# Performance work log

Hardware: AMD Instinct MI355X
Metric: run time of the kernel (lower is better)

## Reference

```python
import jax, jax.numpy as jnp
import numpy as np

NEG_INF = -1e30


def setup_inputs() -> dict:
    key = jax.random.key(0)
    ks = jax.random.split(key, 5)
    B, S, D, H = 2, 2048, 1024, 16
    sc = 0.02  # weight init scale
    return {
        "x": jax.random.normal(ks[0], (B, S, D), dtype=jnp.float32),
        "Wq": jax.random.normal(ks[1], (D, D), dtype=jnp.float32) * sc,
        "bq": jnp.zeros((D,), dtype=jnp.float32),
        "Wk": jax.random.normal(ks[2], (D, D), dtype=jnp.float32) * sc,
        "bk": jnp.zeros((D,), dtype=jnp.float32),
        "Wv": jax.random.normal(ks[3], (D, D), dtype=jnp.float32) * sc,
        "bv": jnp.zeros((D,), dtype=jnp.float32),
        "Wo": jax.random.normal(ks[4], (D, D), dtype=jnp.float32) * sc,
        "bo": jnp.zeros((D,), dtype=jnp.float32),
        "temperature": jnp.ones((H,), dtype=jnp.float32),
    }


def reference(x, Wq, bq, Wk, bk, Wv, bv, Wo, bo, temperature):
    B, S, D = x.shape
    H = temperature.shape[0]
    hd = D // H
    sparsity = 0.8
    k = max(1, int(S * (1.0 - sparsity)))
    scale = hd ** (-0.5)

    # torch Linear: y = x @ W^T + b ; reshape to [B, S, H, hd] -> [B, H, S, hd]
    def proj(W, b):
        return (x @ W.T + b).reshape(B, S, H, hd).transpose(0, 2, 1, 3)

    q, kk, v = proj(Wq, bq), proj(Wk, bk), proj(Wv, bv)

    temp = jnp.clip(temperature, 0.1, None)[None, :, None, None]  # [1,H,1,1]
    scores = jnp.einsum("bhqd,bhkd->bhqk", q, kk) * scale / temp  # [B,H,S,S]

    # top-k sparsity: keep the k largest scores per row, -inf elsewhere.
    # Equivalent to torch's topk+scatter for distinct values: threshold at
    # the k-th largest value per row.
    topk_vals = jax.lax.top_k(scores, k)[0]           # [B,H,S,k]
    kth = topk_vals[..., -1:]                          # [B,H,S,1]
    sparse_scores = jnp.where(scores >= kth, scores, NEG_INF)

    attn = jax.nn.softmax(sparse_scores, axis=-1)      # [B,H,S,S]
    head_out = jnp.einsum("bhqk,bhkd->bhqd", attn, v)  # [B,H,S,hd]

    # stack heads back: [B,S,H,hd] -> [B,S,D], then out projection
    out = head_out.transpose(0, 2, 1, 3).reshape(B, S, D)
    out = out @ Wo.T + bo

    avg_attention = attn.mean(axis=1)                  # [B,S,S]
    return out, avg_attention
```

## Files before the change

kernel.cpp:

```cpp
#include <hip/hip_runtime.h>
#include <stdint.h>

#define S_LEN 2048
#define D_DIM 1024
#define NHEAD 16
#define HD    64
#define TOPK  409

typedef unsigned short u16;
typedef __attribute__((ext_vector_type(8))) short bf16x8;
typedef __attribute__((ext_vector_type(4))) float f32x4;
#define MFMA __builtin_amdgcn_mfma_f32_16x16x32_bf16

__device__ __forceinline__ u16 f2b(float f) {
    unsigned u = __float_as_uint(f);
    return (u16)((u + 0x7fffu + ((u >> 16) & 1u)) >> 16);
}
__device__ __forceinline__ float b2f(u16 h) {
    return __uint_as_float(((unsigned)h) << 16);
}

__global__ __launch_bounds__(256, 4)
void split_f32(const float* __restrict__ src, u16* __restrict__ hi,
               u16* __restrict__ lo, int n4)
{
    const int i = blockIdx.x * 256 + threadIdx.x;
    if (i >= n4) return;
    const float4 v = ((const float4*)src)[i];
    const float vv[4] = {v.x, v.y, v.z, v.w};
    u16 h4[4], l4[4];
#pragma unroll
    for (int c = 0; c < 4; ++c) {
        h4[c] = f2b(vv[c]);
        l4[c] = f2b(vv[c] - b2f(h4[c]));
    }
    ((ushort4*)hi)[i] = make_ushort4(h4[0], h4[1], h4[2], h4[3]);
    ((ushort4*)lo)[i] = make_ushort4(l4[0], l4[1], l4[2], l4[3]);
}

__global__ __launch_bounds__(256, 4)
void split4_f32(const float* __restrict__ s0, const float* __restrict__ s1,
                const float* __restrict__ s2, const float* __restrict__ s3,
                u16* __restrict__ h0, u16* __restrict__ l0,
                u16* __restrict__ h1, u16* __restrict__ l1,
                u16* __restrict__ h2, u16* __restrict__ l2,
                u16* __restrict__ h3, u16* __restrict__ l3, int n4)
{
    const int i = blockIdx.x * 256 + threadIdx.x;
    if (i >= n4) return;
    const int y = blockIdx.y;
    const float* src = (y == 0) ? s0 : (y == 1) ? s1 : (y == 2) ? s2 : s3;
    u16* hi = (y == 0) ? h0 : (y == 1) ? h1 : (y == 2) ? h2 : h3;
    u16* lo = (y == 0) ? l0 : (y == 1) ? l1 : (y == 2) ? l2 : l3;
    const float4 v = ((const float4*)src)[i];
    const float vv[4] = {v.x, v.y, v.z, v.w};
    u16 h4[4], l4[4];
#pragma unroll
    for (int c = 0; c < 4; ++c) {
        h4[c] = f2b(vv[c]);
        l4[c] = f2b(vv[c] - b2f(h4[c]));
    }
    ((ushort4*)hi)[i] = make_ushort4(h4[0], h4[1], h4[2], h4[3]);
    ((ushort4*)lo)[i] = make_ushort4(l4[0], l4[1], l4[2], l4[3]);
}

template<int MODE>
__global__ __launch_bounds__(512, 2)
void proj_mfma(const u16* __restrict__ Ahi, const u16* __restrict__ Alo,
               const u16* __restrict__ Whi, const u16* __restrict__ Wlo,
               const float* __restrict__ bias, float* __restrict__ outf,
               u16* __restrict__ o1, u16* __restrict__ o2)
{
    const int t = threadIdx.x, w = t >> 6, l = t & 63;
    const int lq = l & 15, quad = l >> 4;
    const int m0 = blockIdx.y * 128 + (w >> 2) * 64;
    const int n0 = blockIdx.x * 128 + (w & 3) * 32;

    f32x4 acc[4][2];
#pragma unroll
    for (int i = 0; i < 4; ++i)
#pragma unroll
        for (int j = 0; j < 2; ++j) acc[i][j] = (f32x4){0.f, 0.f, 0.f, 0.f};

    const size_t abase = (size_t)(m0 + lq) * D_DIM + quad * 8;
    const size_t bbase = (size_t)(n0 + lq) * D_DIM + quad * 8;

#pragma unroll 2
    for (int k0 = 0; k0 < D_DIM; k0 += 32) {
        bf16x8 ah[4], al[4], bh[2], bl[2];
#pragma unroll
        for (int i = 0; i < 4; ++i) {
            ah[i] = *(const bf16x8*)(Ahi + abase + (size_t)i * 16 * D_DIM + k0);
            al[i] = *(const bf16x8*)(Alo + abase + (size_t)i * 16 * D_DIM + k0);
        }
#pragma unroll
        for (int j = 0; j < 2; ++j) {
            bh[j] = *(const bf16x8*)(Whi + bbase + (size_t)j * 16 * D_DIM + k0);
            bl[j] = *(const bf16x8*)(Wlo + bbase + (size_t)j * 16 * D_DIM + k0);
        }
#pragma unroll
        for (int i = 0; i < 4; ++i)
#pragma unroll
            for (int j = 0; j < 2; ++j) {
                acc[i][j] = MFMA(ah[i], bh[j], acc[i][j], 0, 0, 0);
                acc[i][j] = MFMA(ah[i], bl[j], acc[i][j], 0, 0, 0);
                acc[i][j] = MFMA(al[i], bh[j], acc[i][j], 0, 0, 0);
            }
    }

#pragma unroll
    for (int j = 0; j < 2; ++j) {
        const int n = n0 + j * 16 + lq;
        const float bb = bias[n];
        const int hh = n >> 6, ee = n & 63;
#pragma unroll
        for (int i = 0; i < 4; ++i) {
            const int mb = m0 + i * 16 + quad * 4;
            const int bbm = mb >> 11, ss = mb & 2047;
            if (MODE == 2) {
#pragma unroll
                for (int r = 0; r < 4; ++r)
                    outf[(size_t)(mb + r) * D_DIM + n] = acc[i][j][r] + bb;
            } else if (MODE == 1) {
                ushort4 pk;
                pk.x = f2b(acc[i][j][0] + bb);
                pk.y = f2b(acc[i][j][1] + bb);
                pk.z = f2b(acc[i][j][2] + bb);
                pk.w = f2b(acc[i][j][3] + bb);
                *(ushort4*)(o1 + ((size_t)((bbm * NHEAD + hh) * HD + ee)) * S_LEN + ss) = pk;
            } else {
#pragma unroll
                for (int r = 0; r < 4; ++r) {
                    const float v = acc[i][j][r] + bb;
                    const size_t idx = ((size_t)(bbm * NHEAD + hh) * S_LEN + ss + r) * HD + ee;
                    const u16 h = f2b(v);
                    o1[idx] = h;
                    o2[idx] = f2b(v - b2f(h));
                }
            }
        }
    }
}

__global__ __launch_bounds__(512, 2)
void attn_mfma(const u16* __restrict__ Qhi, const u16* __restrict__ Qlo,
               const u16* __restrict__ Khi, const u16* __restrict__ Klo,
               const u16* __restrict__ Vt,  const float* __restrict__ temp,
               u16* __restrict__ HOhi, u16* __restrict__ HOlo,
               float* __restrict__ avg)
{
    __shared__ __align__(16) u16 aLds[16 * 2056];
    __shared__ float pvpart[4 * 16 * 16];
    __shared__ int   cnts[16][8][5];
    __shared__ float red[16][8][2];
    __shared__ float rowMu[16], rowSig[16], rowLo[16], rowHi[16], rowZi[16];

    const int t = threadIdx.x, w = t >> 6, l = t & 63;
    const int lq = l & 15, quad = l >> 4;
    const int b  = blockIdx.x >> 7;
    const int q0 = (blockIdx.x & 127) << 4;

    float avgreg[64];
#pragma unroll
    for (int i = 0; i < 64; ++i) avgreg[i] = 0.f;

#pragma unroll 1
    for (int h = 0; h < NHEAD; ++h) {
        const size_t bh = (size_t)(b * NHEAD + h) * S_LEN;
        const float tscale = 0.125f / fmaxf(temp[h], 0.1f);

        const u16* qph = Qhi + (bh + q0 + lq) * HD + quad * 8;
        const u16* qpl = Qlo + (bh + q0 + lq) * HD + quad * 8;
        const bf16x8 qh0 = *(const bf16x8*)qph;
        const bf16x8 qh1 = *(const bf16x8*)(qph + 32);
        const bf16x8 ql0 = *(const bf16x8*)qpl;
        const bf16x8 ql1 = *(const bf16x8*)(qpl + 32);

        f32x4 acc[16];
        const u16* kph = Khi + (bh + w * 256 + lq) * HD + quad * 8;
        const u16* kpl = Klo + (bh + w * 256 + lq) * HD + quad * 8;
#pragma unroll
        for (int tt = 0; tt < 16; ++tt) {
            const bf16x8 k0 = *(const bf16x8*)(kph + tt * 16 * HD);
            const bf16x8 k1 = *(const bf16x8*)(kph + tt * 16 * HD + 32);
            const bf16x8 m0 = *(const bf16x8*)(kpl + tt * 16 * HD);
            const bf16x8 m1 = *(const bf16x8*)(kpl + tt * 16 * HD + 32);
            f32x4 a = {0.f, 0.f, 0.f, 0.f};
            a = MFMA(qh0, k0, a, 0, 0, 0);
            a = MFMA(qh1, k1, a, 0, 0, 0);
            a = MFMA(qh0, m0, a, 0, 0, 0);
            a = MFMA(qh1, m1, a, 0, 0, 0);
            a = MFMA(ql0, k0, a, 0, 0, 0);
            a = MFMA(ql1, k1, a, 0, 0, 0);
            acc[tt] = a * tscale;
        }
        __syncthreads();

        {
            float s1[4] = {0.f,0.f,0.f,0.f}, s2[4] = {0.f,0.f,0.f,0.f};
#pragma unroll
            for (int tt = 0; tt < 16; ++tt)
#pragma unroll
                for (int r = 0; r < 4; ++r) {
                    const float v = acc[tt][r];
                    s1[r] += v;
                    s2[r] = __fmaf_rn(v, v, s2[r]);
                }
#pragma unroll
            for (int off = 1; off < 16; off <<= 1)
#pragma unroll
                for (int r = 0; r < 4; ++r) {
                    s1[r] += __shfl_xor(s1[r], off, 16);
                    s2[r] += __shfl_xor(s2[r], off, 16);
                }
            if (lq == 0)
#pragma unroll
                for (int r = 0; r < 4; ++r) {
                    red[quad * 4 + r][w][0] = s1[r];
                    red[quad * 4 + r][w][1] = s2[r];
                }
        }
        __syncthreads();
        if (t < 16) {
            float a = 0.f, c = 0.f;
#pragma unroll
            for (int ww = 0; ww < 8; ++ww) { a += red[t][ww][0]; c += red[t][ww][1]; }
            const float mu = a * (1.f / 2048.f);
            const float va = c * (1.f / 2048.f) - mu * mu;
            rowMu[t] = mu;
            rowSig[t] = sqrtf(fmaxf(va, 0.f));
        }
        __syncthreads();

        {
            float th[5][4];
            int c[5][4];
#pragma unroll
            for (int r = 0; r < 4; ++r) {
                const float mu = rowMu[quad * 4 + r], sg = rowSig[quad * 4 + r];
#pragma unroll
                for (int i = 0; i < 5; ++i) {
                    th[i][r] = __fmaf_rn(sg, 0.55f + 0.15f * (float)i, mu);
                    c[i][r] = 0;
                }
            }
#pragma unroll
            for (int tt = 0; tt < 16; ++tt)
#pragma unroll
                for (int r = 0; r < 4; ++r) {
                    const float v = acc[tt][r];
#pragma unroll
                    for (int i = 0; i < 5; ++i) c[i][r] += (v >= th[i][r]) ? 1 : 0;
                }
#pragma unroll
            for (int off = 1; off < 16; off <<= 1)
#pragma unroll
                for (int i = 0; i < 5; ++i)
#pragma unroll
                    for (int r = 0; r < 4; ++r) c[i][r] += __shfl_xor(c[i][r], off, 16);
            if (lq == 0)
#pragma unroll
                for (int r = 0; r < 4; ++r)
#pragma unroll
                    for (int i = 0; i < 5; ++i) cnts[quad * 4 + r][w][i] = c[i][r];
        }
        __syncthreads();
        if (t < 16) {
            int c[5] = {0, 0, 0, 0, 0};
#pragma unroll
            for (int ww = 0; ww < 8; ++ww)
#pragma unroll
                for (int i = 0; i < 5; ++i) c[i] += cnts[t][ww][i];
            const float mu = rowMu[t], sg = rowSig[t];
            float lo, hi;
            if (c[0] < TOPK) {
                lo = __fmaf_rn(sg, -6.f, mu);
                hi = __fmaf_rn(sg, 0.55f + 0.15f * 0.f, mu);
            } else if (c[4] >= TOPK) {
                lo = __fmaf_rn(sg, 0.55f + 0.15f * 4.f, mu);
                hi = __fmaf_rn(sg, 6.f, mu);
            } else {
                int bi = 0;
#pragma unroll
                for (int j = 1; j < 4; ++j) if (c[j] >= TOPK) bi = j;
                lo = __fmaf_rn(sg, 0.55f + 0.15f * (float)bi, mu);
                hi = __fmaf_rn(sg, 0.55f + 0.15f * (float)(bi + 1), mu);
            }
            rowLo[t] = lo;
            rowHi[t] = hi;
        }
        __syncthreads();

#pragma unroll 1
        for (int rd = 0; rd < 5; ++rd) {
            {
                float th[3][4];
                int c[3][4];
#pragma unroll
                for (int r = 0; r < 4; ++r) {
                    const float lo_ = rowLo[quad * 4 + r], hi_ = rowHi[quad * 4 + r];
                    const float w4 = __fmul_rn(__fsub_rn(hi_, lo_), 0.25f);
#pragma unroll
                    for (int j = 0; j < 3; ++j) {
                        th[j][r] = __fmaf_rn(w4, (float)(j + 1), lo_);
                        c[j][r] = 0;
                    }
                }
#pragma unroll
                for (int tt = 0; tt < 16; ++tt)
#pragma unroll
                    for (int r = 0; r < 4; ++r) {
                        const float v = acc[tt][r];
#pragma unroll
                        for (int j = 0; j < 3; ++j) c[j][r] += (v >= th[j][r]) ? 1 : 0;
                    }
#pragma unroll
                for (int off = 1; off < 16; off <<= 1)
#pragma unroll
                    for (int j = 0; j < 3; ++j)
#pragma unroll
                        for (int r = 0; r < 4; ++r) c[j][r] += __shfl_xor(c[j][r], off, 16);
                if (lq == 0)
#pragma unroll
                    for (int r = 0; r < 4; ++r)
#pragma unroll
                        for (int j = 0; j < 3; ++j) cnts[quad * 4 + r][w][j] = c[j][r];
            }
            __syncthreads();
            if (t < 16) {
                int d[3] = {0, 0, 0};
#pragma unroll
                for (int ww = 0; ww < 8; ++ww)
#pragma unroll
                    for (int j = 0; j < 3; ++j) d[j] += cnts[t][ww][j];
                float lo = rowLo[t], hi = rowHi[t];
                const float w4 = __fmul_rn(__fsub_rn(hi, lo), 0.25f);
                const float t1 = __fmaf_rn(w4, 1.f, lo);
                const float t2 = __fmaf_rn(w4, 2.f, lo);
                const float t3 = __fmaf_rn(w4, 3.f, lo);
                if (d[2] >= TOPK)      { lo = t3; }
                else if (d[1] >= TOPK) { lo = t2; hi = t3; }
                else if (d[0] >= TOPK) { lo = t1; hi = t2; }
                else                   { hi = t1; }
                rowLo[t] = lo;
                rowHi[t] = hi;
            }
            __syncthreads();
        }

        float kth[4], zp[4] = {0.f, 0.f, 0.f, 0.f};
#pragma unroll
        for (int r = 0; r < 4; ++r) kth[r] = rowLo[quad * 4 + r];
#pragma unroll
        for (int tt = 0; tt < 16; ++tt)
#pragma unroll
            for (int r = 0; r < 4; ++r) {
                const float v = acc[tt][r];
                const float e = (v >= kth[r]) ? __expf(v) : 0.f;
                acc[tt][r] = e;
                zp[r] += e;
            }
#pragma unroll
        for (int off = 1; off < 16; off <<= 1)
#pragma unroll
            for (int r = 0; r < 4; ++r) zp[r] += __shfl_xor(zp[r], off, 16);
        if (lq == 0)
#pragma unroll
            for (int r = 0; r < 4; ++r) red[quad * 4 + r][w][0] = zp[r];
        __syncthreads();
        if (t < 16) {
            float z = 0.f;
#pragma unroll
            for (int ww = 0; ww < 8; ++ww) z += red[t][ww][0];
            rowZi[t] = 1.f / z;
        }
        __syncthreads();
        float zi[4];
#pragma unroll
        for (int r = 0; r < 4; ++r) zi[r] = rowZi[quad * 4 + r];

#pragma unroll
        for (int tt = 0; tt < 16; ++tt)
#pragma unroll
            for (int r = 0; r < 4; ++r) {
                const float a_ = acc[tt][r] * zi[r];
                avgreg[tt * 4 + r] += a_;
                aLds[(quad * 4 + r) * 2056 + w * 256 + tt * 16 + lq] = f2b(a_);
            }
        __syncthreads();

        const int et = w & 3, jh = w >> 2;
        const u16* vb = Vt + ((size_t)(b * NHEAD + h) * HD + et * 16 + lq) * S_LEN
                        + jh * 1024 + quad * 8;
        const u16* ab = aLds + lq * 2056 + jh * 1024 + quad * 8;
        f32x4 pv = {0.f, 0.f, 0.f, 0.f};
#pragma unroll 8
        for (int st = 0; st < 32; ++st) {
            const bf16x8 af = *(const bf16x8*)(ab + st * 32);
            const bf16x8 vf = *(const bf16x8*)(vb + st * 32);
            pv = MFMA(af, vf, pv, 0, 0, 0);
        }
        if (w >= 4) {
#pragma unroll
            for (int r = 0; r < 4; ++r)
                pvpart[(et * 16 + quad * 4 + r) * 16 + lq] = pv[r];
        }
        __syncthreads();
        if (w < 4) {
#pragma unroll
            for (int r = 0; r < 4; ++r) {
                const float v = pv[r] + pvpart[(et * 16 + quad * 4 + r) * 16 + lq];
                const size_t idx =
                    ((size_t)(b * S_LEN + q0 + quad * 4 + r)) * D_DIM + h * HD + et * 16 + lq;
                const u16 hv = f2b(v);
                HOhi[idx] = hv;
                HOlo[idx] = f2b(v - b2f(hv));
            }
        }
    }

#pragma unroll
    for (int tt = 0; tt < 16; ++tt)
#pragma unroll
        for (int r = 0; r < 4; ++r)
            avg[((size_t)(b * S_LEN + q0 + quad * 4 + r)) * S_LEN + w * 256 + tt * 16 + lq] =
                avgreg[tt * 4 + r] * (1.f / NHEAD);
}

extern "C" void kernel_launch(void* const* d_in, const int* in_sizes, int n_in,
                              void* d_out, int out_size, void* d_ws, size_t ws_size,
                              hipStream_t stream)
{
    const float* x    = (const float*)d_in[0];
    const float* Wq   = (const float*)d_in[1];
    const float* bq   = (const float*)d_in[2];
    const float* Wk   = (const float*)d_in[3];
    const float* bk   = (const float*)d_in[4];
    const float* Wv   = (const float*)d_in[5];
    const float* bv   = (const float*)d_in[6];
    const float* Wo   = (const float*)d_in[7];
    const float* bo   = (const float*)d_in[8];
    const float* temp = (const float*)d_in[9];
    float* out = (float*)d_out;

    const int B = in_sizes[0] / (S_LEN * D_DIM);
    const int M = B * S_LEN;
    const size_t NQ = (size_t)M * D_DIM;
    const size_t NW = (size_t)D_DIM * D_DIM;

    u16* Qhi = (u16*)d_ws;
    u16* Qlo = Qhi + NQ;
    u16* Khi = Qlo + NQ;
    u16* Klo = Khi + NQ;
    u16* Vt  = Klo + NQ;
    u16* Xhi = Vt  + NQ;
    u16* Xlo = Xhi + NQ;
    u16* Wqh = Xlo + NQ;
    u16* Wql = Wqh + NW;
    u16* Wkh = Wql + NW;
    u16* Wkl = Wkh + NW;
    u16* Wvh = Wkl + NW;
    u16* Wvl = Wvh + NW;
    u16* Woh = Wvl + NW;
    u16* Wol = Woh + NW;
    float* avg = out + NQ;

    const int n4x = (int)(NQ / 4), n4w = (int)(NW / 4);
    split_f32<<<(n4x + 255) / 256, 256, 0, stream>>>(x, Xhi, Xlo, n4x);
    split4_f32<<<dim3((n4w + 255) / 256, 4), 256, 0, stream>>>(
        Wq, Wk, Wv, Wo, Wqh, Wql, Wkh, Wkl, Wvh, Wvl, Woh, Wol, n4w);

    dim3 gg(D_DIM / 128, M / 128, 1);
    proj_mfma<0><<<gg, 512, 0, stream>>>(Xhi, Xlo, Wqh, Wql, bq, nullptr, Qhi, Qlo);
    proj_mfma<0><<<gg, 512, 0, stream>>>(Xhi, Xlo, Wkh, Wkl, bk, nullptr, Khi, Klo);
    proj_mfma<1><<<gg, 512, 0, stream>>>(Xhi, Xlo, Wvh, Wvl, bv, nullptr, Vt, nullptr);

    attn_mfma<<<dim3(M / 16), 512, 0, stream>>>(Qhi, Qlo, Khi, Klo, Vt, temp,
                                                Xhi, Xlo, avg);

    proj_mfma<2><<<gg, 512, 0, stream>>>(Xhi, Xlo, Woh, Wol, bo, out, nullptr, nullptr);
}
```

Before: 1.180 ms.

## Transpose scores through LDS so each half-wave owns a row, removing block barriers

```diff
diff --git a/kernel.cpp b/kernel.cpp
--- a/kernel.cpp
+++ b/kernel.cpp
@@ -149,16 +149,15 @@
                u16* __restrict__ HOhi, u16* __restrict__ HOlo,
                float* __restrict__ avg)
 {
-    __shared__ __align__(16) u16 aLds[16 * 2056];
+    __shared__ __align__(16) float sLds[16 * 2060];
     __shared__ float pvpart[4 * 16 * 16];
-    __shared__ int   cnts[16][8][5];
-    __shared__ float red[16][8][2];
-    __shared__ float rowMu[16], rowSig[16], rowLo[16], rowHi[16], rowZi[16];
 
     const int t = threadIdx.x, w = t >> 6, l = t & 63;
     const int lq = l & 15, quad = l >> 4;
+    const int hl = l & 31, rhalf = l >> 5;
     const int b  = blockIdx.x >> 7;
     const int q0 = (blockIdx.x & 127) << 4;
+    const int myrow = 2 * w + rhalf;
 
     float avgreg[64];
 #pragma unroll
@@ -194,205 +193,127 @@
             a = MFMA(ql1, k1, a, 0, 0, 0);
             acc[tt] = a * tscale;
         }
+
+#pragma unroll
+        for (int tt = 0; tt < 16; ++tt)
+#pragma unroll
+            for (int r = 0; r < 4; ++r)
+                sLds[(quad * 4 + r) * 2060 + w * 256 + tt * 16 + lq] = acc[tt][r];
         __syncthreads();
 
+        float s[64];
         {
-            float s1[4] = {0.f,0.f,0.f,0.f}, s2[4] = {0.f,0.f,0.f,0.f};
-#pragma unroll
-            for (int tt = 0; tt < 16; ++tt)
-#pragma unroll
-                for (int r = 0; r < 4; ++r) {
-                    const float v = acc[tt][r];
-                    s1[r] += v;
-                    s2[r] = __fmaf_rn(v, v, s2[r]);
-                }
-#pragma unroll
-            for (int off = 1; off < 16; off <<= 1)
-#pragma unroll
-                for (int r = 0; r < 4; ++r) {
-                    s1[r] += __shfl_xor(s1[r], off, 16);
-                    s2[r] += __shfl_xor(s2[r], off, 16);
-                }
-            if (lq == 0)
-#pragma unroll
-                for (int r = 0; r < 4; ++r) {
-                    red[quad * 4 + r][w][0] = s1[r];
-                    red[quad * 4 + r][w][1] = s2[r];
-                }
-        }
-        __syncthreads();
-        if (t < 16) {
-            float a = 0.f, c = 0.f;
-#pragma unroll
-            for (int ww = 0; ww < 8; ++ww) { a += red[t][ww][0]; c += red[t][ww][1]; }
-            const float mu = a * (1.f / 2048.f);
-            const float va = c * (1.f / 2048.f) - mu * mu;
-            rowMu[t] = mu;
-            rowSig[t] = sqrtf(fmaxf(va, 0.f));
-        }
-        __syncthreads();
-
+            const float* srow = sLds + (size_t)myrow * 2060 + 2 * hl;
+#pragma unroll
+            for (int j = 0; j < 32; ++j) {
+                const float2 p = *(const float2*)(srow + 64 * j);
+                s[2 * j]     = p.x;
+                s[2 * j + 1] = p.y;
+            }
+        }
+
+        float s1 = 0.f, s2 = 0.f;
+#pragma unroll
+        for (int j = 0; j < 64; ++j) { s1 += s[j]; s2 = __fmaf_rn(s[j], s[j], s2); }
+#pragma unroll
+        for (int off = 1; off < 32; off <<= 1) {
+            s1 += __shfl_xor(s1, off, 32);
+            s2 += __shfl_xor(s2, off, 32);
+        }
+        const float mu = s1 * (1.f / 2048.f);
+        const float va = s2 * (1.f / 2048.f) - mu * mu;
+        const float sg = sqrtf(fmaxf(va, 0.f));
+
+        float lo, hi;
         {
-            float th[5][4];
-            int c[5][4];
-#pragma unroll
-            for (int r = 0; r < 4; ++r) {
-                const float mu = rowMu[quad * 4 + r], sg = rowSig[quad * 4 + r];
-#pragma unroll
-                for (int i = 0; i < 5; ++i) {
-                    th[i][r] = __fmaf_rn(sg, 0.55f + 0.15f * (float)i, mu);
-                    c[i][r] = 0;
-                }
-            }
-#pragma unroll
-            for (int tt = 0; tt < 16; ++tt)
-#pragma unroll
-                for (int r = 0; r < 4; ++r) {
-                    const float v = acc[tt][r];
-#pragma unroll
-                    for (int i = 0; i < 5; ++i) c[i][r] += (v >= th[i][r]) ? 1 : 0;
-                }
-#pragma unroll
-            for (int off = 1; off < 16; off <<= 1)
-#pragma unroll
-                for (int i = 0; i < 5; ++i)
-#pragma unroll
-                    for (int r = 0; r < 4; ++r) c[i][r] += __shfl_xor(c[i][r], off, 16);
-            if (lq == 0)
-#pragma unroll
-                for (int r = 0; r < 4; ++r)
-#pragma unroll
-                    for (int i = 0; i < 5; ++i) cnts[quad * 4 + r][w][i] = c[i][r];
-        }
-        __syncthreads();
-        if (t < 16) {
-            int c[5] = {0, 0, 0, 0, 0};
-#pragma unroll
-            for (int ww = 0; ww < 8; ++ww)
-#pragma unroll
-                for (int i = 0; i < 5; ++i) c[i] += cnts[t][ww][i];
-            const float mu = rowMu[t], sg = rowSig[t];
-            float lo, hi;
+            float th[5];
+            int c[5];
+#pragma unroll
+            for (int i = 0; i < 5; ++i) {
+                th[i] = __fmaf_rn(sg, 0.55f + 0.15f * (float)i, mu);
+                c[i] = 0;
+            }
+#pragma unroll
+            for (int j = 0; j < 64; ++j) {
+                const float v = s[j];
+#pragma unroll
+                for (int i = 0; i < 5; ++i) c[i] += (v >= th[i]) ? 1 : 0;
+            }
+#pragma unroll
+            for (int off = 1; off < 32; off <<= 1)
+#pragma unroll
+                for (int i = 0; i < 5; ++i) c[i] += __shfl_xor(c[i], off, 32);
             if (c[0] < TOPK) {
                 lo = __fmaf_rn(sg, -6.f, mu);
-                hi = __fmaf_rn(sg, 0.55f + 0.15f * 0.f, mu);
+                hi = th[0];
             } else if (c[4] >= TOPK) {
-                lo = __fmaf_rn(sg, 0.55f + 0.15f * 4.f, mu);
+                lo = th[4];
                 hi = __fmaf_rn(sg, 6.f, mu);
             } else {
                 int bi = 0;
 #pragma unroll
                 for (int j = 1; j < 4; ++j) if (c[j] >= TOPK) bi = j;
-                lo = __fmaf_rn(sg, 0.55f + 0.15f * (float)bi, mu);
-                hi = __fmaf_rn(sg, 0.55f + 0.15f * (float)(bi + 1), mu);
-            }
-            rowLo[t] = lo;
-            rowHi[t] = hi;
-        }
-        __syncthreads();
+                lo = th[bi];
+                hi = th[bi + 1];
+            }
+        }
 
 #pragma unroll 1
         for (int rd = 0; rd < 5; ++rd) {
-            {
-                float th[3][4];
-                int c[3][4];
-#pragma unroll
-                for (int r = 0; r < 4; ++r) {
-                    const float lo_ = rowLo[quad * 4 + r], hi_ = rowHi[quad * 4 + r];
-                    const float w4 = __fmul_rn(__fsub_rn(hi_, lo_), 0.25f);
-#pragma unroll
-                    for (int j = 0; j < 3; ++j) {
-                        th[j][r] = __fmaf_rn(w4, (float)(j + 1), lo_);
-                        c[j][r] = 0;
-                    }
-                }
-#pragma unroll
-                for (int tt = 0; tt < 16; ++tt)
-#pragma unroll
-                    for (int r = 0; r < 4; ++r) {
-                        const float v = acc[tt][r];
-#pragma unroll
-                        for (int j = 0; j < 3; ++j) c[j][r] += (v >= th[j][r]) ? 1 : 0;
-                    }
-#pragma unroll
-                for (int off = 1; off < 16; off <<= 1)
-#pragma unroll
-                    for (int j = 0; j < 3; ++j)
-#pragma unroll
-                        for (int r = 0; r < 4; ++r) c[j][r] += __shfl_xor(c[j][r], off, 16);
-                if (lq == 0)
-#pragma unroll
-                    for (int r = 0; r < 4; ++r)
-#pragma unroll
-                        for (int j = 0; j < 3; ++j) cnts[quad * 4 + r][w][j] = c[j][r];
-            }
-            __syncthreads();
-            if (t < 16) {
-                int d[3] = {0, 0, 0};
-#pragma unroll
-                for (int ww = 0; ww < 8; ++ww)
-#pragma unroll
-                    for (int j = 0; j < 3; ++j) d[j] += cnts[t][ww][j];
-                float lo = rowLo[t], hi = rowHi[t];
-                const float w4 = __fmul_rn(__fsub_rn(hi, lo), 0.25f);
-                const float t1 = __fmaf_rn(w4, 1.f, lo);
-                const float t2 = __fmaf_rn(w4, 2.f, lo);
-                const float t3 = __fmaf_rn(w4, 3.f, lo);
-                if (d[2] >= TOPK)      { lo = t3; }
-                else if (d[1] >= TOPK) { lo = t2; hi = t3; }
-                else if (d[0] >= TOPK) { lo = t1; hi = t2; }
-                else                   { hi = t1; }
-                rowLo[t] = lo;
-                rowHi[t] = hi;
-            }
-            __syncthreads();
-        }
-
-        float kth[4], zp[4] = {0.f, 0.f, 0.f, 0.f};
-#pragma unroll
-        for (int r = 0; r < 4; ++r) kth[r] = rowLo[quad * 4 + r];
-#pragma unroll
-        for (int tt = 0; tt < 16; ++tt)
-#pragma unroll
-            for (int r = 0; r < 4; ++r) {
-                const float v = acc[tt][r];
-                const float e = (v >= kth[r]) ? __expf(v) : 0.f;
-                acc[tt][r] = e;
-                zp[r] += e;
-            }
-#pragma unroll
-        for (int off = 1; off < 16; off <<= 1)
-#pragma unroll
-            for (int r = 0; r < 4; ++r) zp[r] += __shfl_xor(zp[r], off, 16);
-        if (lq == 0)
-#pragma unroll
-            for (int r = 0; r < 4; ++r) red[quad * 4 + r][w][0] = zp[r];
-        __syncthreads();
-        if (t < 16) {
-            float z = 0.f;
-#pragma unroll
-            for (int ww = 0; ww < 8; ++ww) z += red[t][ww][0];
-            rowZi[t] = 1.f / z;
-        }
-        __syncthreads();
-        float zi[4];
-#pragma unroll
-        for (int r = 0; r < 4; ++r) zi[r] = rowZi[quad * 4 + r];
-
-#pragma unroll
-        for (int tt = 0; tt < 16; ++tt)
-#pragma unroll
-            for (int r = 0; r < 4; ++r) {
-                const float a_ = acc[tt][r] * zi[r];
-                avgreg[tt * 4 + r] += a_;
-                aLds[(quad * 4 + r) * 2056 + w * 256 + tt * 16 + lq] = f2b(a_);
-            }
+            const float w4 = __fmul_rn(__fsub_rn(hi, lo), 0.25f);
+            const float t1 = __fmaf_rn(w4, 1.f, lo);
+            const float t2 = __fmaf_rn(w4, 2.f, lo);
+            const float t3 = __fmaf_rn(w4, 3.f, lo);
+            int d0 = 0, d1 = 0, d2 = 0;
+#pragma unroll
+            for (int j = 0; j < 64; ++j) {
+                const float v = s[j];
+                d0 += (v >= t1) ? 1 : 0;
+                d1 += (v >= t2) ? 1 : 0;
+                d2 += (v >= t3) ? 1 : 0;
+            }
+#pragma unroll
+            for (int off = 1; off < 32; off <<= 1) {
+                d0 += __shfl_xor(d0, off, 32);
+                d1 += __shfl_xor(d1, off, 32);
+                d2 += __shfl_xor(d2, off, 32);
+            }
+            if (d2 >= TOPK)      { lo = t3; }
+            else if (d1 >= TOPK) { lo = t2; hi = t3; }
+            else if (d0 >= TOPK) { lo = t1; hi = t2; }
+            else                 { hi = t1; }
+        }
+
+        const float kth = lo;
+        float zp = 0.f;
+#pragma unroll
+        for (int j = 0; j < 64; ++j) {
+            const float e = (s[j] >= kth) ? __expf(s[j]) : 0.f;
+            s[j] = e;
+            zp += e;
+        }
+#pragma unroll
+        for (int off = 1; off < 32; off <<= 1) zp += __shfl_xor(zp, off, 32);
+        const float zi = 1.f / zp;
+
+        {
+            u16* arow = (u16*)(sLds + (size_t)myrow * 2060);
+#pragma unroll
+            for (int j = 0; j < 32; ++j) {
+                const float a0 = s[2 * j] * zi;
+                const float a1 = s[2 * j + 1] * zi;
+                avgreg[2 * j]     += a0;
+                avgreg[2 * j + 1] += a1;
+                const unsigned pk = (unsigned)f2b(a0) | ((unsigned)f2b(a1) << 16);
+                *(unsigned*)(arow + 2 * hl + 64 * j) = pk;
+            }
+        }
         __syncthreads();
 
         const int et = w & 3, jh = w >> 2;
         const u16* vb = Vt + ((size_t)(b * NHEAD + h) * HD + et * 16 + lq) * S_LEN
                         + jh * 1024 + quad * 8;
-        const u16* ab = aLds + lq * 2056 + jh * 1024 + quad * 8;
+        const u16* ab = (const u16*)sLds + (size_t)lq * 4120 + jh * 1024 + quad * 8;
         f32x4 pv = {0.f, 0.f, 0.f, 0.f};
 #pragma unroll 8
         for (int st = 0; st < 32; ++st) {
@@ -419,12 +340,14 @@
         }
     }
 
-#pragma unroll
-    for (int tt = 0; tt < 16; ++tt)
-#pragma unroll
-        for (int r = 0; r < 4; ++r)
-            avg[((size_t)(b * S_LEN + q0 + quad * 4 + r)) * S_LEN + w * 256 + tt * 16 + lq] =
-                avgreg[tt * 4 + r] * (1.f / NHEAD);
+    float* avrow = avg + ((size_t)(b * S_LEN + q0 + myrow)) * S_LEN + 2 * hl;
+#pragma unroll
+    for (int j = 0; j < 32; ++j) {
+        float2 o;
+        o.x = avgreg[2 * j]     * (1.f / NHEAD);
+        o.y = avgreg[2 * j + 1] * (1.f / NHEAD);
+        *(float2*)(avrow + 64 * j) = o;
+    }
 }
 
 extern "C" void kernel_launch(void* const* d_in, const int* in_sizes, int n_in,
```

New measurement: 1.060 ms. -10.2%, faster.
